# Optimization experiments

Hardware: AMD Instinct MI355X
Metric: run time of the kernel (lower is better)

The kernel has to match this reference:

```python
import jax, jax.numpy as jnp
import numpy as np

OCC_THRESHOLD = 0.5  # occupancy-bitfield stand-in: cell occupied if grid value > 0.5
T_CLAMP = 1e10


def setup_inputs() -> dict:
    key = jax.random.key(0)
    k1, k2, k3 = jax.random.split(key, 3)
    R = 65536
    # origins inside the scene box [-1,1]^3 (uniform in [-0.5,0.5]^3)
    rays_o = jax.random.uniform(k1, (R, 3), dtype=jnp.float32) - 0.5
    d = jax.random.normal(k2, (R, 3), dtype=jnp.float32)
    rays_d = d / jnp.linalg.norm(d, axis=-1, keepdims=True)
    aabb = jnp.array([[-1.0, -1.0, -1.0], [1.0, 1.0, 1.0]], dtype=jnp.float32)
    density_grid = jax.random.uniform(k3, (1, 128, 128, 128), dtype=jnp.float32)
    return {"rays_o": rays_o, "rays_d": rays_d, "aabb": aabb,
            "density_grid": density_grid, "num_samples": 128}


def reference(rays_o, rays_d, aabb, density_grid, num_samples):
    R = rays_o.shape[0]
    S = int(num_samples)
    aabb_min, aabb_max = aabb[0], aabb[1]

    # ---- ray-AABB intersection (slab test), matching nerfactory_cuda.ray_aabb_intersect ----
    inv_d = 1.0 / rays_d
    t0 = (aabb_min - rays_o) * inv_d  # [R,3]
    t1 = (aabb_max - rays_o) * inv_d
    tn = jnp.max(jnp.minimum(t0, t1), axis=-1)
    tf = jnp.min(jnp.maximum(t0, t1), axis=-1)
    tn = jnp.maximum(tn, 0.0)
    miss = tf <= tn
    t_min = jnp.minimum(jnp.where(miss, T_CLAMP, tn), T_CLAMP)  # [R]
    t_max = jnp.minimum(jnp.where(miss, T_CLAMP, tf), T_CLAMP)  # [R]

    # ---- raymarching: S uniform steps in [t_min, t_max], keep occupied cells ----
    dt = jnp.where(miss, 0.0, (t_max - t_min) / S)  # [R]
    i = jnp.arange(S, dtype=rays_o.dtype)
    starts = t_min[:, None] + i * dt[:, None]        # [R,S]
    ends = starts + dt[:, None]
    t_mid = 0.5 * (starts + ends)
    pos = rays_o[:, None, :] + rays_d[:, None, :] * t_mid[..., None]  # [R,S,3]

    res = density_grid.shape[-1]
    u = (pos - aabb_min) / (aabb_max - aabb_min)  # normalized [0,1]
    cell = jnp.clip(jnp.floor(u * res).astype(jnp.int32), 0, res - 1)
    occ = density_grid[0, cell[..., 0], cell[..., 1], cell[..., 2]] > OCC_THRESHOLD
    valid = occ & (~miss[:, None]) & (dt[:, None] > 0)  # [R,S]

    # ---- stream compaction into packed buffer (fixed capacity R*S) ----
    total = R * S
    flat_valid = valid.reshape(-1)
    excl = jnp.cumsum(flat_valid.astype(jnp.int32)) - flat_valid.astype(jnp.int32)
    scatter_idx = jnp.where(flat_valid, excl, total)  # invalid -> dummy slot

    origins_b = jnp.broadcast_to(rays_o[:, None, :], (R, S, 3))
    dirs_b = jnp.broadcast_to(rays_d[:, None, :], (R, S, 3))
    vals = jnp.concatenate(
        [origins_b, dirs_b, starts[..., None], ends[..., None]], axis=-1
    ).reshape(total, 8)
    packed = jnp.zeros((total + 1, 8), dtype=vals.dtype).at[scatter_idx].set(vals)[:total]

    counts = valid.sum(axis=-1).astype(jnp.int32)        # samples per ray
    ray_start = jnp.cumsum(counts) - counts              # exclusive cumsum
    packed_info = jnp.stack([ray_start, counts], axis=-1)  # [R,2]

    # packed columns: origins(0:3), dirs(3:6), starts(6), ends(7)
    return packed, packed_info, t_min, t_max
```

## Files before the change

kernel.cpp:

```cpp
#include <hip/hip_runtime.h>

#define SAMPLES 128
#define GRID_RES 128

typedef unsigned long long u64;

__device__ __forceinline__ void slab_test(
    float ox, float oy, float oz, float dx, float dy, float dz,
    float a0, float a1, float a2, float b0, float b1, float b2,
    float& tmin, float& tmax, float& dtv, bool& miss)
{
    float ix = __fdiv_rn(1.0f, dx);
    float iy = __fdiv_rn(1.0f, dy);
    float iz = __fdiv_rn(1.0f, dz);
    float t0x = __fmul_rn(__fsub_rn(a0, ox), ix);
    float t1x = __fmul_rn(__fsub_rn(b0, ox), ix);
    float t0y = __fmul_rn(__fsub_rn(a1, oy), iy);
    float t1y = __fmul_rn(__fsub_rn(b1, oy), iy);
    float t0z = __fmul_rn(__fsub_rn(a2, oz), iz);
    float t1z = __fmul_rn(__fsub_rn(b2, oz), iz);
    float tn = fmaxf(fmaxf(fminf(t0x, t1x), fminf(t0y, t1y)), fminf(t0z, t1z));
    float tf = fminf(fminf(fmaxf(t0x, t1x), fmaxf(t0y, t1y)), fmaxf(t0z, t1z));
    tn = fmaxf(tn, 0.0f);
    miss = (tf <= tn);
    tmin = miss ? 1e10f : fminf(tn, 1e10f);
    tmax = miss ? 1e10f : fminf(tf, 1e10f);
    dtv  = miss ? 0.0f : __fdiv_rn(__fsub_rn(tmax, tmin), (float)SAMPLES);
}

__global__ __launch_bounds__(256) void k_bits(
    const float* __restrict__ grid, u64* __restrict__ bits, int ncells)
{
    int c = blockIdx.x * 256 + threadIdx.x;
    bool occ = (c < ncells) && (grid[c] > 0.5f);
    u64 m = __ballot(occ);
    if ((threadIdx.x & 63) == 0 && c < ncells) bits[c >> 6] = m;
}

__global__ __launch_bounds__(256) void k_ray(
    const float* __restrict__ ro, const float* __restrict__ rd,
    const float* __restrict__ aabb,
    float* __restrict__ out_tmin, float* __restrict__ out_tmax,
    float* __restrict__ wtmin, float* __restrict__ wdt, int R)
{
    int r = blockIdx.x * 256 + threadIdx.x;
    if (r >= R) return;
    float ox = ro[3 * r + 0], oy = ro[3 * r + 1], oz = ro[3 * r + 2];
    float dx = rd[3 * r + 0], dy = rd[3 * r + 1], dz = rd[3 * r + 2];
    float a0 = aabb[0], a1 = aabb[1], a2 = aabb[2];
    float b0 = aabb[3], b1 = aabb[4], b2 = aabb[5];
    float tmin, tmax, dtv; bool miss;
    slab_test(ox, oy, oz, dx, dy, dz, a0, a1, a2, b0, b1, b2,
              tmin, tmax, dtv, miss);
    out_tmin[r] = tmin;
    out_tmax[r] = tmax;
    wtmin[r] = tmin;
    wdt[r]  = dtv;
}

__global__ __launch_bounds__(256) void k_pass1(
    const float* __restrict__ ro, const float* __restrict__ rd,
    const float* __restrict__ aabb, const u64* __restrict__ bits,
    const float* __restrict__ wtmin, const float* __restrict__ wdt,
    u64* __restrict__ wmask, int R)
{
    int tid = threadIdx.x;
    int ray = blockIdx.x * 2 + (tid >> 7);
    int s   = tid & 127;
    if (ray >= R) return;
    int rayu = __builtin_amdgcn_readfirstlane(ray);

    float tmin = wtmin[rayu];
    float dtv  = wdt[rayu];

    bool valid = false;
    if (dtv > 0.0f) {
        float ox = ro[3 * rayu + 0], oy = ro[3 * rayu + 1], oz = ro[3 * rayu + 2];
        float dx = rd[3 * rayu + 0], dy = rd[3 * rayu + 1], dz = rd[3 * rayu + 2];
        float a0 = aabb[0], a1 = aabb[1], a2 = aabb[2];
        float b0 = aabb[3], b1 = aabb[4], b2 = aabb[5];

        float fs    = (float)s;
        float start = __fadd_rn(tmin, __fmul_rn(fs, dtv));
        float end   = __fadd_rn(start, dtv);
        float tmid  = __fmul_rn(0.5f, __fadd_rn(start, end));
        float px = __fadd_rn(ox, __fmul_rn(dx, tmid));
        float py = __fadd_rn(oy, __fmul_rn(dy, tmid));
        float pz = __fadd_rn(oz, __fmul_rn(dz, tmid));
        float e0 = __fsub_rn(b0, a0);
        float e1 = __fsub_rn(b1, a1);
        float e2 = __fsub_rn(b2, a2);
        float ux = __fmul_rn(__fdiv_rn(__fsub_rn(px, a0), e0), (float)GRID_RES);
        float uy = __fmul_rn(__fdiv_rn(__fsub_rn(py, a1), e1), (float)GRID_RES);
        float uz = __fmul_rn(__fdiv_rn(__fsub_rn(pz, a2), e2), (float)GRID_RES);
        int cx = min(max((int)floorf(ux), 0), GRID_RES - 1);
        int cy = min(max((int)floorf(uy), 0), GRID_RES - 1);
        int cz = min(max((int)floorf(uz), 0), GRID_RES - 1);
        int idx = ((cx * GRID_RES) + cy) * GRID_RES + cz;
        valid = (bits[idx >> 6] >> (idx & 63)) & 1ull;
    }

    u64 bmask = __ballot(valid);
    if ((tid & 63) == 0) {
        wmask[(size_t)ray * 2 + (s >> 6)] = bmask;
    }
}

__global__ __launch_bounds__(1024) void k_scanA(
    const u64* __restrict__ wmask, unsigned* __restrict__ lpre,
    unsigned* __restrict__ bsum, int R)
{
    int r    = blockIdx.x * 1024 + threadIdx.x;
    int lane = threadIdx.x & 63;
    int wv   = threadIdx.x >> 6;

    unsigned c = 0;
    if (r < R)
        c = (unsigned)__popcll(wmask[2 * r]) + (unsigned)__popcll(wmask[2 * r + 1]);

    unsigned inc = c;
    for (int o = 1; o < 64; o <<= 1) {
        unsigned v = __shfl_up(inc, o, 64);
        if (lane >= o) inc += v;
    }

    __shared__ unsigned sw[16];
    if (lane == 63) sw[wv] = inc;
    __syncthreads();
    if (wv == 0) {
        unsigned v = (lane < 16) ? sw[lane] : 0u;
        unsigned iv = v;
        for (int o = 1; o < 16; o <<= 1) {
            unsigned t2 = __shfl_up(iv, o, 64);
            if (lane >= o) iv += t2;
        }
        if (lane < 16) sw[lane] = iv - v;
    }
    __syncthreads();

    unsigned excl = sw[wv] + (inc - c);
    if (r < R) lpre[r] = excl;
    if (threadIdx.x == 1023) bsum[blockIdx.x] = excl + c;
}

__global__ __launch_bounds__(64) void k_scanB(
    const unsigned* __restrict__ bsum, unsigned* __restrict__ boff,
    unsigned* __restrict__ wtotal, int nb)
{
    int t = threadIdx.x;
    unsigned v = (t < nb) ? bsum[t] : 0u;
    unsigned iv = v;
    for (int o = 1; o < 64; o <<= 1) {
        unsigned u = __shfl_up(iv, o, 64);
        if (t >= o) iv += u;
    }
    if (t < nb) boff[t] = iv - v;
    if (t == 63) *wtotal = iv;
}

__global__ __launch_bounds__(256) void k_pack(
    const float* __restrict__ ro, const float* __restrict__ rd,
    const u64* __restrict__ wmask,
    const unsigned* __restrict__ lpre, const unsigned* __restrict__ boff,
    const float* __restrict__ wtmin, const float* __restrict__ wdt,
    const unsigned* __restrict__ wtotal,
    float* __restrict__ packed, float* __restrict__ info, int R)
{
    int gid = blockIdx.x * blockDim.x + threadIdx.x;
    if (gid >= R * SAMPLES) return;
    int ray = gid >> 7;
    int s   = gid & 127;
    int rayu = __builtin_amdgcn_readfirstlane(ray);

    u64 mlo = wmask[2 * rayu];
    u64 mhi = wmask[2 * rayu + 1];
    unsigned wstart = boff[rayu >> 10] + lpre[rayu];

    if (s == 0) {
        unsigned cnt = (unsigned)__popcll(mlo) + (unsigned)__popcll(mhi);
        info[2 * ray]     = (float)wstart;
        info[2 * ray + 1] = (float)cnt;
    }

    bool valid;
    unsigned below;
    if (s < 64) {
        valid = (mlo >> s) & 1ull;
        below = (unsigned)__popcll(mlo & ((1ull << s) - 1ull));
    } else {
        int s2 = s - 64;
        valid = (mhi >> s2) & 1ull;
        below = (unsigned)__popcll(mlo) +
                (unsigned)__popcll(mhi & ((1ull << s2) - 1ull));
    }

    unsigned vex = wstart + below;
    unsigned row;
    float4 v0, v1;
    if (valid) {
        row = vex;
        float tmin = wtmin[rayu];
        float dtv  = wdt[rayu];
        float fs    = (float)s;
        float start = __fadd_rn(tmin, __fmul_rn(fs, dtv));
        float end   = __fadd_rn(start, dtv);
        v0 = make_float4(ro[3 * rayu + 0], ro[3 * rayu + 1], ro[3 * rayu + 2],
                         rd[3 * rayu + 0]);
        v1 = make_float4(rd[3 * rayu + 1], rd[3 * rayu + 2], start, end);
    } else {
        row = *wtotal + ((unsigned)gid - vex);
        v0 = make_float4(0.f, 0.f, 0.f, 0.f);
        v1 = v0;
    }
    float4* p = (float4*)(packed + (size_t)row * 8);
    p[0] = v0;
    p[1] = v1;
}

extern "C" void kernel_launch(void* const* d_in, const int* in_sizes, int n_in,
                              void* d_out, int out_size, void* d_ws, size_t ws_size,
                              hipStream_t stream)
{
    const float* ro   = (const float*)d_in[0];
    const float* rd   = (const float*)d_in[1];
    const float* aabb = (const float*)d_in[2];
    const float* grid = (const float*)d_in[3];

    int R = in_sizes[0] / 3;
    size_t total = (size_t)R * SAMPLES;
    int nb = (R + 1023) / 1024;
    int ncells = GRID_RES * GRID_RES * GRID_RES;

    float* out    = (float*)d_out;
    float* packed = out;
    float* info   = out + total * 8;
    float* otmin  = info + (size_t)2 * R;
    float* otmax  = otmin + R;

    char* w = (char*)d_ws;
    u64* wmask       = (u64*)w;
    float* wtmin     = (float*)(w + (size_t)R * 16);
    float* wdt       = wtmin + R;
    unsigned* lpre   = (unsigned*)(wdt + R);
    unsigned* bsum   = lpre + R;
    unsigned* boff   = bsum + 64;
    unsigned* wtotal = boff + 64;
    u64* bits        = (u64*)(wtotal + 63);

    k_bits<<<(ncells + 255) / 256, 256, 0, stream>>>(grid, bits, ncells);
    int b0 = (R + 255) / 256;
    k_ray<<<b0, 256, 0, stream>>>(ro, rd, aabb, otmin, otmax, wtmin, wdt, R);
    int b1 = (R + 1) / 2;
    k_pass1<<<b1, 256, 0, stream>>>(ro, rd, aabb, bits, wtmin, wdt, wmask, R);
    k_scanA<<<nb, 1024, 0, stream>>>(wmask, lpre, bsum, R);
    k_scanB<<<1, 64, 0, stream>>>(bsum, boff, wtotal, nb);
    int b3 = (int)((total + 255) / 256);
    k_pack<<<b3, 256, 0, stream>>>(ro, rd, wmask, lpre, boff, wtmin, wdt,
                                   wtotal, packed, info, R);
}
```

Baseline: 93.01 us.

## Merge prep kernels and fold block-sum scan into last-block-done scan kernel

Combines the occupancy-bitfield and ray slab-test kernels into one launch that dispatches by block index. It also removes the separate single-block scan kernel: each scan block atomically publishes its sum and bumps a counter, and the last block to finish computes the block offsets and total. This cuts two kernel launches and their inter-kernel gaps, at the cost of atomics, fences and a counter that must be reset every call. The ctr slot sits in the padding just after wtotal.

```diff
diff --git a/kernel.cpp b/kernel.cpp
--- a/kernel.cpp
+++ b/kernel.cpp
@@ -28,22 +28,25 @@
     dtv  = miss ? 0.0f : __fdiv_rn(__fsub_rn(tmax, tmin), (float)SAMPLES);
 }
 
-__global__ __launch_bounds__(256) void k_bits(
-    const float* __restrict__ grid, u64* __restrict__ bits, int ncells)
-{
-    int c = blockIdx.x * 256 + threadIdx.x;
-    bool occ = (c < ncells) && (grid[c] > 0.5f);
-    u64 m = __ballot(occ);
-    if ((threadIdx.x & 63) == 0 && c < ncells) bits[c >> 6] = m;
-}
-
-__global__ __launch_bounds__(256) void k_ray(
+__global__ __launch_bounds__(256) void k_prep(
+    const float* __restrict__ grid, u64* __restrict__ bits, int ncells,
     const float* __restrict__ ro, const float* __restrict__ rd,
     const float* __restrict__ aabb,
     float* __restrict__ out_tmin, float* __restrict__ out_tmax,
-    float* __restrict__ wtmin, float* __restrict__ wdt, int R)
-{
-    int r = blockIdx.x * 256 + threadIdx.x;
+    float* __restrict__ wtmin, float* __restrict__ wdt,
+    unsigned* __restrict__ ctr, int R, int nbb)
+{
+    int b = blockIdx.x;
+    int tid = threadIdx.x;
+    if (b < nbb) {
+        int c = b * 256 + tid;
+        bool occ = (c < ncells) && (grid[c] > 0.5f);
+        u64 m = __ballot(occ);
+        if ((tid & 63) == 0 && c < ncells) bits[c >> 6] = m;
+        return;
+    }
+    int r = (b - nbb) * 256 + tid;
+    if (b == nbb && tid == 0) *ctr = 0u;
     if (r >= R) return;
     float ox = ro[3 * r + 0], oy = ro[3 * r + 1], oz = ro[3 * r + 2];
     float dx = rd[3 * r + 0], dy = rd[3 * r + 1], dz = rd[3 * r + 2];
@@ -106,9 +109,11 @@
     }
 }
 
-__global__ __launch_bounds__(1024) void k_scanA(
+__global__ __launch_bounds__(1024) void k_scan(
     const u64* __restrict__ wmask, unsigned* __restrict__ lpre,
-    unsigned* __restrict__ bsum, int R)
+    unsigned* __restrict__ bsum, unsigned* __restrict__ boff,
+    unsigned* __restrict__ wtotal, unsigned* __restrict__ ctr,
+    int R, int nb)
 {
     int r    = blockIdx.x * 1024 + threadIdx.x;
     int lane = threadIdx.x & 63;
@@ -125,6 +130,7 @@
     }
 
     __shared__ unsigned sw[16];
+    __shared__ unsigned sdone;
     if (lane == 63) sw[wv] = inc;
     __syncthreads();
     if (wv == 0) {
@@ -140,22 +146,27 @@
 
     unsigned excl = sw[wv] + (inc - c);
     if (r < R) lpre[r] = excl;
-    if (threadIdx.x == 1023) bsum[blockIdx.x] = excl + c;
-}
-
-__global__ __launch_bounds__(64) void k_scanB(
-    const unsigned* __restrict__ bsum, unsigned* __restrict__ boff,
-    unsigned* __restrict__ wtotal, int nb)
-{
-    int t = threadIdx.x;
-    unsigned v = (t < nb) ? bsum[t] : 0u;
-    unsigned iv = v;
-    for (int o = 1; o < 64; o <<= 1) {
-        unsigned u = __shfl_up(iv, o, 64);
-        if (t >= o) iv += u;
-    }
-    if (t < nb) boff[t] = iv - v;
-    if (t == 63) *wtotal = iv;
+
+    if (threadIdx.x == 1023) {
+        atomicExch(&bsum[blockIdx.x], excl + c);
+        __threadfence();
+        sdone = atomicAdd(ctr, 1u);
+    }
+    __syncthreads();
+    if (sdone == (unsigned)(nb - 1)) {
+        __threadfence();
+        if (threadIdx.x < 64) {
+            int t = threadIdx.x;
+            unsigned v = (t < nb) ? atomicAdd(&bsum[t], 0u) : 0u;
+            unsigned iv = v;
+            for (int o = 1; o < 64; o <<= 1) {
+                unsigned u = __shfl_up(iv, o, 64);
+                if (t >= o) iv += u;
+            }
+            if (t < nb) boff[t] = iv - v;
+            if (t == 63) *wtotal = iv;
+        }
+    }
 }
 
 __global__ __launch_bounds__(256) void k_pack(
@@ -230,6 +241,8 @@
     size_t total = (size_t)R * SAMPLES;
     int nb = (R + 1023) / 1024;
     int ncells = GRID_RES * GRID_RES * GRID_RES;
+    int nbb = (ncells + 255) / 256;
+    int nrb = (R + 255) / 256;
 
     float* out    = (float*)d_out;
     float* packed = out;
@@ -245,15 +258,14 @@
     unsigned* bsum   = lpre + R;
     unsigned* boff   = bsum + 64;
     unsigned* wtotal = boff + 64;
+    unsigned* ctr    = wtotal + 1;
     u64* bits        = (u64*)(wtotal + 63);
 
-    k_bits<<<(ncells + 255) / 256, 256, 0, stream>>>(grid, bits, ncells);
-    int b0 = (R + 255) / 256;
-    k_ray<<<b0, 256, 0, stream>>>(ro, rd, aabb, otmin, otmax, wtmin, wdt, R);
+    k_prep<<<nbb + nrb, 256, 0, stream>>>(grid, bits, ncells, ro, rd, aabb,
+                                          otmin, otmax, wtmin, wdt, ctr, R, nbb);
     int b1 = (R + 1) / 2;
     k_pass1<<<b1, 256, 0, stream>>>(ro, rd, aabb, bits, wtmin, wdt, wmask, R);
-    k_scanA<<<nb, 1024, 0, stream>>>(wmask, lpre, bsum, R);
-    k_scanB<<<1, 64, 0, stream>>>(bsum, boff, wtotal, nb);
+    k_scan<<<nb, 1024, 0, stream>>>(wmask, lpre, bsum, boff, wtotal, ctr, R, nb);
     int b3 = (int)((total + 255) / 256);
     k_pack<<<b3, 256, 0, stream>>>(ro, rd, wmask, lpre, boff, wtmin, wdt,
                                    wtotal, packed, info, R);
```

Result: no change. 94.22 us (+1.3%).
